# Kernel optimization log

Measured on AMD Instinct MI355X. Metric: run time of the kernel, lower is better.

Reference implementation:

```python
import jax, jax.numpy as jnp
import numpy as np
from jax import lax

OUT_SCALE = 0.001


def setup_inputs() -> dict:
    key = jax.random.key(0)
    kz, kx = jax.random.split(key)
    z = jax.random.normal(kz, (64, 256, 7, 7), dtype=jnp.float32)
    x = jax.random.normal(kx, (64, 256, 31, 31), dtype=jnp.float32)
    return {"z": z, "x": x}


def reference(z, x):
    # depthwise cross-correlation: each (batch, channel) slice of z is slid
    # over the matching slice of x. Implemented as a grouped conv with
    # feature_group_count = B*C, exactly mirroring torch F.conv2d(groups=B*C).
    B, C, kh, kw = z.shape
    H, W = x.shape[2], x.shape[3]
    x_r = x.reshape(1, B * C, H, W)           # [1, B*C, H, W]
    k_r = z.reshape(B * C, 1, kh, kw)          # [B*C, 1, kh, kw] (OIHW)
    out = lax.conv_general_dilated(
        x_r, k_r,
        window_strides=(1, 1),
        padding="VALID",
        feature_group_count=B * C,
        dimension_numbers=("NCHW", "OIHW", "NCHW"),
    )  # [1, B*C, H-kh+1, W-kw+1]
    out = out.reshape(B, C, out.shape[2], out.shape[3])
    return out * OUT_SCALE
```

## Files before the change

kernel.cpp:

```cpp
#include <hip/hip_runtime.h>


#define KH 7
#define KW 7
#define XW 31
#define OH 25
#define OW 25
#define NSLICE (64 * 256)
#define THREADS 128
#define NBLK 2560
#define NWAVES (NBLK * 2)
#define BUF_DW 1024
#define SLICE_X (XW * XW)
#define SLICE_O (OH * OW)
#define X_TOTAL_DW (NSLICE * SLICE_X)

__device__ __forceinline__ void gl_lds16(const float* g, float* l) {
    __builtin_amdgcn_global_load_lds(
        (const __attribute__((address_space(1))) void*)g,
        (__attribute__((address_space(3))) void*)l, 16, 0, 0);
}

__device__ __forceinline__ void stage_slice(const float* __restrict__ x,
                                            float* __restrict__ buf,
                                            int slice, int lane) {
    const int g0 = (slice * SLICE_X) & ~3;
    #pragma unroll
    for (int k = 0; k < 4; ++k) {
        const int dw = k * 256 + lane * 4;
        gl_lds16(x + min(g0 + dw, X_TOTAL_DW - 4), buf + dw);
    }
}

__device__ __forceinline__ void process_slice(float* __restrict__ buf,
                                              const float* __restrict__ z,
                                              float* __restrict__ out,
                                              int slice, int lane,
                                              int oy, int c0, bool act) {
    const int pre = (slice * SLICE_X) & 3;
    const float* __restrict__ zw = z + (size_t)slice * (KH * KW);
    if (act) {
        float acc[13] = {};
        const float* __restrict__ xrow = buf + pre;
        #pragma unroll
        for (int i = 0; i < KH; ++i) {
            const float* __restrict__ p = xrow + (oy + i) * XW + c0;
            float f[19];
            #pragma unroll
            for (int c = 0; c < 19; ++c) f[c] = p[c];
            #pragma unroll
            for (int j = 0; j < KW; ++j) {
                const float w = zw[i * KW + j];
                #pragma unroll
                for (int c = 0; c < 13; ++c)
                    acc[c] = fmaf(f[c + j], w, acc[c]);
            }
        }
        const int fb = oy * OW + c0;
        #pragma unroll
        for (int c = 0; c < 12; ++c) buf[fb + c] = acc[c] * 0.001f;
        if (c0 == 0) buf[fb + 12] = acc[12] * 0.001f;
    }
    float* __restrict__ og = out + (size_t)slice * SLICE_O;
    #pragma unroll
    for (int k = 0; k < 9; ++k) og[k * 64 + lane] = buf[k * 64 + lane];
    if (lane < SLICE_O - 576) og[576 + lane] = buf[576 + lane];
}

__global__ __launch_bounds__(THREADS, 5)
void xcorr_dw_kernel(const float* __restrict__ z,
                     const float* __restrict__ x,
                     float* __restrict__ out) {
    __shared__ float xs[2][2][BUF_DW];
    const int lane = threadIdx.x & 63;
    const int wv   = __builtin_amdgcn_readfirstlane(threadIdx.x >> 6);
    const int wid  = blockIdx.x * 2 + wv;

    const int h   = (lane >= OH) ? 1 : 0;
    const int oy  = h ? lane - OH : lane;
    const int c0  = h ? 13 : 0;
    const bool act = (lane < 2 * OH);

    float* bcur = xs[wv][0];
    float* bnxt = xs[wv][1];

    stage_slice(x, bcur, wid, lane);
    stage_slice(x, bnxt, wid + NWAVES, lane);

    asm volatile("s_waitcnt vmcnt(4)" ::: "memory");
    __builtin_amdgcn_sched_barrier(0);
    process_slice(bcur, z, out, wid, lane, oy, c0, act);
    asm volatile("s_waitcnt lgkmcnt(0)" ::: "memory");
    __builtin_amdgcn_sched_barrier(0);
    {
        const int s2 = wid + 2 * NWAVES;
        stage_slice(x, bcur, s2 < NSLICE ? s2 : 0, lane);
    }
    { float* t = bcur; bcur = bnxt; bnxt = t; }

    #pragma unroll 1
    for (int p = wid + NWAVES; p < NSLICE; p += NWAVES) {
        asm volatile("s_waitcnt vmcnt(14)" ::: "memory");
        __builtin_amdgcn_sched_barrier(0);
        process_slice(bcur, z, out, p, lane, oy, c0, act);
        asm volatile("s_waitcnt lgkmcnt(0)" ::: "memory");
        __builtin_amdgcn_sched_barrier(0);
        const int s2 = p + 2 * NWAVES;
        stage_slice(x, bcur, s2 < NSLICE ? s2 : 0, lane);
        float* t = bcur; bcur = bnxt; bnxt = t;
    }

    asm volatile("s_waitcnt vmcnt(0)" ::: "memory");
}

extern "C" void kernel_launch(void* const* d_in, const int* in_sizes, int n_in,
                              void* d_out, int out_size, void* d_ws, size_t ws_size,
                              hipStream_t stream) {
    const float* z = (const float*)d_in[0];
    const float* x = (const float*)d_in[1];
    float* out = (float*)d_out;
    xcorr_dw_kernel<<<dim3(NBLK), dim3(THREADS), 0, stream>>>(z, x, out);
}
```

Baseline: 116.2 us.

## Replace async global-to-LDS double buffering with register-staged prefetch per wave

Drops the direct global_load_lds double-buffered persistent loop. Each wave now handles four consecutive slices, prefetching the next slice into registers while the current one is processed, then writing it into a single LDS buffer. This halves LDS use per block and removes the hand-tuned waitcnt sequencing. The cost is more VGPRs for the staged data, a lower occupancy hint (4 instead of 5), and many more blocks with a less persistent schedule.

```diff
diff --git a/kernel.cpp b/kernel.cpp
--- a/kernel.cpp
+++ b/kernel.cpp
@@ -8,28 +8,33 @@
 #define OW 25
 #define NSLICE (64 * 256)
 #define THREADS 128
-#define NBLK 2560
-#define NWAVES (NBLK * 2)
+#define SPW 4
+#define NBLK (NSLICE / (2 * SPW))
 #define BUF_DW 1024
 #define SLICE_X (XW * XW)
 #define SLICE_O (OH * OW)
 #define X_TOTAL_DW (NSLICE * SLICE_X)
 
-__device__ __forceinline__ void gl_lds16(const float* g, float* l) {
-    __builtin_amdgcn_global_load_lds(
-        (const __attribute__((address_space(1))) void*)g,
-        (__attribute__((address_space(3))) void*)l, 16, 0, 0);
+__device__ __forceinline__ void load_slice_regs(const float* __restrict__ x,
+                                                int slice, int lane,
+                                                float4& r0, float4& r1,
+                                                float4& r2, float4& r3) {
+    const int g0 = (slice * SLICE_X) & ~3;
+    const int l4 = lane * 4;
+    r0 = *reinterpret_cast<const float4*>(x + min(g0 + 0 * 256 + l4, X_TOTAL_DW - 4));
+    r1 = *reinterpret_cast<const float4*>(x + min(g0 + 1 * 256 + l4, X_TOTAL_DW - 4));
+    r2 = *reinterpret_cast<const float4*>(x + min(g0 + 2 * 256 + l4, X_TOTAL_DW - 4));
+    r3 = *reinterpret_cast<const float4*>(x + min(g0 + 3 * 256 + l4, X_TOTAL_DW - 4));
 }
 
-__device__ __forceinline__ void stage_slice(const float* __restrict__ x,
-                                            float* __restrict__ buf,
-                                            int slice, int lane) {
-    const int g0 = (slice * SLICE_X) & ~3;
-    #pragma unroll
-    for (int k = 0; k < 4; ++k) {
-        const int dw = k * 256 + lane * 4;
-        gl_lds16(x + min(g0 + dw, X_TOTAL_DW - 4), buf + dw);
-    }
+__device__ __forceinline__ void write_slice_lds(float* __restrict__ buf, int lane,
+                                                const float4& r0, const float4& r1,
+                                                const float4& r2, const float4& r3) {
+    const int l4 = lane * 4;
+    *reinterpret_cast<float4*>(buf + 0 * 256 + l4) = r0;
+    *reinterpret_cast<float4*>(buf + 1 * 256 + l4) = r1;
+    *reinterpret_cast<float4*>(buf + 2 * 256 + l4) = r2;
+    *reinterpret_cast<float4*>(buf + 3 * 256 + l4) = r3;
 }
 
 __device__ __forceinline__ void process_slice(float* __restrict__ buf,
@@ -67,50 +72,35 @@
     if (lane < SLICE_O - 576) og[576 + lane] = buf[576 + lane];
 }
 
-__global__ __launch_bounds__(THREADS, 5)
+__global__ __launch_bounds__(THREADS, 4)
 void xcorr_dw_kernel(const float* __restrict__ z,
                      const float* __restrict__ x,
                      float* __restrict__ out) {
-    __shared__ float xs[2][2][BUF_DW];
+    __shared__ float xs[2][BUF_DW];
     const int lane = threadIdx.x & 63;
     const int wv   = __builtin_amdgcn_readfirstlane(threadIdx.x >> 6);
+    float* __restrict__ buf = xs[wv];
+
     const int wid  = blockIdx.x * 2 + wv;
+    const int base = wid * SPW;
 
     const int h   = (lane >= OH) ? 1 : 0;
     const int oy  = h ? lane - OH : lane;
     const int c0  = h ? 13 : 0;
     const bool act = (lane < 2 * OH);
 
-    float* bcur = xs[wv][0];
-    float* bnxt = xs[wv][1];
+    float4 r0, r1, r2, r3;
 
-    stage_slice(x, bcur, wid, lane);
-    stage_slice(x, bnxt, wid + NWAVES, lane);
+    load_slice_regs(x, base, lane, r0, r1, r2, r3);
+    write_slice_lds(buf, lane, r0, r1, r2, r3);
 
-    asm volatile("s_waitcnt vmcnt(4)" ::: "memory");
-    __builtin_amdgcn_sched_barrier(0);
-    process_slice(bcur, z, out, wid, lane, oy, c0, act);
-    asm volatile("s_waitcnt lgkmcnt(0)" ::: "memory");
-    __builtin_amdgcn_sched_barrier(0);
-    {
-        const int s2 = wid + 2 * NWAVES;
-        stage_slice(x, bcur, s2 < NSLICE ? s2 : 0, lane);
+    #pragma unroll
+    for (int i = 0; i < SPW; ++i) {
+        const int s = base + i;
+        if (i + 1 < SPW) load_slice_regs(x, s + 1, lane, r0, r1, r2, r3);
+        process_slice(buf, z, out, s, lane, oy, c0, act);
+        if (i + 1 < SPW) write_slice_lds(buf, lane, r0, r1, r2, r3);
     }
-    { float* t = bcur; bcur = bnxt; bnxt = t; }
-
-    #pragma unroll 1
-    for (int p = wid + NWAVES; p < NSLICE; p += NWAVES) {
-        asm volatile("s_waitcnt vmcnt(14)" ::: "memory");
-        __builtin_amdgcn_sched_barrier(0);
-        process_slice(bcur, z, out, p, lane, oy, c0, act);
-        asm volatile("s_waitcnt lgkmcnt(0)" ::: "memory");
-        __builtin_amdgcn_sched_barrier(0);
-        const int s2 = p + 2 * NWAVES;
-        stage_slice(x, bcur, s2 < NSLICE ? s2 : 0, lane);
-        float* t = bcur; bcur = bnxt; bnxt = t;
-    }
-
-    asm volatile("s_waitcnt vmcnt(0)" ::: "memory");
 }
 
 extern "C" void kernel_launch(void* const* d_in, const int* in_sizes, int n_in,
```

Result: slower. 121.0 us (+4.1%).

## Warp-specialize blocks: one loader wave stages three slices for three compute waves

Applied to the files above, without the earlier changes.

The kernel moves from per-wave self-staged double buffering to a 4-wave block where wave 3 is a dedicated producer. That wave copies three contiguous x slices into a shared LDS half-buffer with global_load_lds, and the other three waves each compute one slice. Rounds are synchronized with block barriers over a two-buffer ping-pong, and each block covers 12 slices in 4 rounds. The aim is larger contiguous loads and separating memory issue from FMA work. In exchange, a quarter of the waves do no compute, and only one stage of prefetch is in flight behind a full vmcnt(0) wait plus a block barrier each round, which may reduce latency hiding.

```diff
diff --git a/kernel.cpp b/kernel.cpp
--- a/kernel.cpp
+++ b/kernel.cpp
@@ -7,10 +7,10 @@
 #define OH 25
 #define OW 25
 #define NSLICE (64 * 256)
-#define THREADS 128
-#define NBLK 2560
-#define NWAVES (NBLK * 2)
-#define BUF_DW 1024
+#define THREADS 256
+#define NBLK 1536
+#define RND 4
+#define HALF_DW 3072
 #define SLICE_X (XW * XW)
 #define SLICE_O (OH * OW)
 #define X_TOTAL_DW (NSLICE * SLICE_X)
@@ -21,96 +21,81 @@
         (__attribute__((address_space(3))) void*)l, 16, 0, 0);
 }
 
-__device__ __forceinline__ void stage_slice(const float* __restrict__ x,
-                                            float* __restrict__ buf,
-                                            int slice, int lane) {
-    const int g0 = (slice * SLICE_X) & ~3;
+__device__ __forceinline__ void stage3(const float* __restrict__ x,
+                                       float* __restrict__ half,
+                                       int sbase, int lane) {
+    const int g0 = (sbase * SLICE_X) & ~3;
     #pragma unroll
-    for (int k = 0; k < 4; ++k) {
+    for (int k = 0; k < 12; ++k) {
         const int dw = k * 256 + lane * 4;
-        gl_lds16(x + min(g0 + dw, X_TOTAL_DW - 4), buf + dw);
+        gl_lds16(x + min(g0 + dw, X_TOTAL_DW - 4), half + dw);
     }
 }
 
-__device__ __forceinline__ void process_slice(float* __restrict__ buf,
-                                              const float* __restrict__ z,
-                                              float* __restrict__ out,
-                                              int slice, int lane,
-                                              int oy, int c0, bool act) {
-    const int pre = (slice * SLICE_X) & 3;
-    const float* __restrict__ zw = z + (size_t)slice * (KH * KW);
-    if (act) {
-        float acc[13] = {};
-        const float* __restrict__ xrow = buf + pre;
-        #pragma unroll
-        for (int i = 0; i < KH; ++i) {
-            const float* __restrict__ p = xrow + (oy + i) * XW + c0;
-            float f[19];
-            #pragma unroll
-            for (int c = 0; c < 19; ++c) f[c] = p[c];
-            #pragma unroll
-            for (int j = 0; j < KW; ++j) {
-                const float w = zw[i * KW + j];
-                #pragma unroll
-                for (int c = 0; c < 13; ++c)
-                    acc[c] = fmaf(f[c + j], w, acc[c]);
-            }
-        }
-        const int fb = oy * OW + c0;
-        #pragma unroll
-        for (int c = 0; c < 12; ++c) buf[fb + c] = acc[c] * 0.001f;
-        if (c0 == 0) buf[fb + 12] = acc[12] * 0.001f;
-    }
-    float* __restrict__ og = out + (size_t)slice * SLICE_O;
-    #pragma unroll
-    for (int k = 0; k < 9; ++k) og[k * 64 + lane] = buf[k * 64 + lane];
-    if (lane < SLICE_O - 576) og[576 + lane] = buf[576 + lane];
-}
-
-__global__ __launch_bounds__(THREADS, 5)
+__global__ __launch_bounds__(THREADS, 6)
 void xcorr_dw_kernel(const float* __restrict__ z,
                      const float* __restrict__ x,
                      float* __restrict__ out) {
-    __shared__ float xs[2][2][BUF_DW];
+    __shared__ float xs[2][HALF_DW];
     const int lane = threadIdx.x & 63;
     const int wv   = __builtin_amdgcn_readfirstlane(threadIdx.x >> 6);
-    const int wid  = blockIdx.x * 2 + wv;
+    const int b    = blockIdx.x;
 
-    const int h   = (lane >= OH) ? 1 : 0;
-    const int oy  = h ? lane - OH : lane;
-    const int c0  = h ? 13 : 0;
-    const bool act = (lane < 2 * OH);
-
-    float* bcur = xs[wv][0];
-    float* bnxt = xs[wv][1];
-
-    stage_slice(x, bcur, wid, lane);
-    stage_slice(x, bnxt, wid + NWAVES, lane);
-
-    asm volatile("s_waitcnt vmcnt(4)" ::: "memory");
-    __builtin_amdgcn_sched_barrier(0);
-    process_slice(bcur, z, out, wid, lane, oy, c0, act);
-    asm volatile("s_waitcnt lgkmcnt(0)" ::: "memory");
-    __builtin_amdgcn_sched_barrier(0);
-    {
-        const int s2 = wid + 2 * NWAVES;
-        stage_slice(x, bcur, s2 < NSLICE ? s2 : 0, lane);
+    if (wv == 3) {
+        stage3(x, xs[0], 12 * b, lane);
+        asm volatile("s_waitcnt vmcnt(0)" ::: "memory");
+        __builtin_amdgcn_sched_barrier(0);
+        #pragma unroll 1
+        for (int r = 0; r < RND; ++r) {
+            __builtin_amdgcn_s_barrier();
+            if (r + 1 < RND) {
+                stage3(x, xs[(r + 1) & 1], 12 * b + 3 * (r + 1), lane);
+                asm volatile("s_waitcnt vmcnt(0)" ::: "memory");
+                __builtin_amdgcn_sched_barrier(0);
+            }
+        }
+    } else {
+        const int h   = (lane >= OH) ? 1 : 0;
+        const int oy  = h ? lane - OH : lane;
+        const int c0  = h ? 13 : 0;
+        const bool act = (lane < 2 * OH);
+        #pragma unroll 1
+        for (int r = 0; r < RND; ++r) {
+            __builtin_amdgcn_s_barrier();
+            const int sbase = 12 * b + 3 * r;
+            const int s     = sbase + wv;
+            if (s < NSLICE) {
+                const int pre = (sbase * SLICE_X) & 3;
+                float* __restrict__ buf = xs[r & 1] + pre + wv * SLICE_X;
+                const float* __restrict__ zw = z + (size_t)s * (KH * KW);
+                if (act) {
+                    float acc[13] = {};
+                    #pragma unroll
+                    for (int i = 0; i < KH; ++i) {
+                        const float* __restrict__ p = buf + (oy + i) * XW + c0;
+                        float f[19];
+                        #pragma unroll
+                        for (int c = 0; c < 19; ++c) f[c] = p[c];
+                        #pragma unroll
+                        for (int j = 0; j < KW; ++j) {
+                            const float w = zw[i * KW + j];
+                            #pragma unroll
+                            for (int c = 0; c < 13; ++c)
+                                acc[c] = fmaf(f[c + j], w, acc[c]);
+                        }
+                    }
+                    const int fb = oy * OW + c0;
+                    #pragma unroll
+                    for (int c = 0; c < 12; ++c) buf[fb + c] = acc[c] * 0.001f;
+                    if (c0 == 0) buf[fb + 12] = acc[12] * 0.001f;
+                }
+                float* __restrict__ og = out + (size_t)s * SLICE_O;
+                #pragma unroll
+                for (int k = 0; k < 9; ++k) og[k * 64 + lane] = buf[k * 64 + lane];
+                if (lane < SLICE_O - 576) og[576 + lane] = buf[576 + lane];
+            }
+        }
     }
-    { float* t = bcur; bcur = bnxt; bnxt = t; }
-
-    #pragma unroll 1
-    for (int p = wid + NWAVES; p < NSLICE; p += NWAVES) {
-        asm volatile("s_waitcnt vmcnt(14)" ::: "memory");
-        __builtin_amdgcn_sched_barrier(0);
-        process_slice(bcur, z, out, p, lane, oy, c0, act);
-        asm volatile("s_waitcnt lgkmcnt(0)" ::: "memory");
-        __builtin_amdgcn_sched_barrier(0);
-        const int s2 = p + 2 * NWAVES;
-        stage_slice(x, bcur, s2 < NSLICE ? s2 : 0, lane);
-        float* t = bcur; bcur = bnxt; bnxt = t;
-    }
-
-    asm volatile("s_waitcnt vmcnt(0)" ::: "memory");
 }
 
 extern "C" void kernel_launch(void* const* d_in, const int* in_sizes, int n_in,
```

New measurement: 116.8 us. Within noise of the previous version (+0.5%).
